# Performance work log

Measured on AMD Instinct MI355X. Metric: run time of the kernel, lower is better.

Reference implementation:

```python
import jax, jax.numpy as jnp
import numpy as np

# static config (matches torch module instantiation)
B, D, NH, HD = 2, 256, 8, 32
NL, NP, DFF = 1, 4, 1024
SHAPES = [(180, 180)]          # (H, W) per level; 180*180 = 32400
STARTS = [0]
LSRC = 32400
N_DET, N_SEG = 200, 100        # SEG_QUERY_NUM=100 -> num_seg_query=300
LQ = N_DET + N_SEG


def _lin(key, dout, din, scale=None):
    scale = scale if scale is not None else 1.0 / np.sqrt(din)
    k1, k2 = jax.random.split(key)
    return (jax.random.normal(k1, (dout, din), jnp.float32) * scale,
            jax.random.normal(k2, (dout,), jnp.float32) * 0.01)


def setup_inputs() -> dict:
    key = jax.random.key(0)
    ks = iter(jax.random.split(key, 64))
    inp = {
        'query': jax.random.normal(next(ks), (B, LQ, D), jnp.float32),
        'query_pos': jax.random.normal(next(ks), (B, LQ, D), jnp.float32),
        'src': jax.random.normal(next(ks), (B, LSRC, D), jnp.float32),
        'pos': jax.random.normal(next(ks), (B, LSRC, D), jnp.float32),
        'reference_points': jax.random.uniform(next(ks), (B, LSRC + LQ, NL, 2), jnp.float32),
        'spatial_shapes': jnp.array(SHAPES, jnp.int32),
        'level_start_index': jnp.array(STARTS, jnp.int32),
    }
    # two MSDeformAttn instances (self_attn = sa_*, cross_attn = ca_*)
    for pre in ('sa', 'ca'):
        inp[pre + '_Wv'], inp[pre + '_bv'] = _lin(next(ks), D, D)
        inp[pre + '_Woff'], inp[pre + '_boff'] = _lin(next(ks), NH * NL * NP * 2, D, scale=0.01)
        inp[pre + '_Waw'], inp[pre + '_baw'] = _lin(next(ks), NH * NL * NP, D, scale=0.01)
        inp[pre + '_Wout'], inp[pre + '_bout'] = _lin(next(ks), D, D)
    for nm in ('norm1', 'norm2', 'normq', 'qa_norm', 'norm3'):
        inp[nm + '_g'] = jnp.ones((D,), jnp.float32)
        inp[nm + '_b'] = jnp.zeros((D,), jnp.float32)
    inp['ffn1_W1'], inp['ffn1_b1'] = _lin(next(ks), DFF, D)
    inp['ffn1_W2'], inp['ffn1_b2'] = _lin(next(ks), D, DFF)
    inp['ffn3_W1'], inp['ffn3_b1'] = _lin(next(ks), DFF, D)
    inp['ffn3_W2'], inp['ffn3_b2'] = _lin(next(ks), D, DFF)
    # TCSLayer: proj(d->2d) then gate1/gate2 (d->d), sigmoid gates
    inp['tcs_Wp'], inp['tcs_bp'] = _lin(next(ks), 2 * D, D)
    inp['tcs_Wg1'], inp['tcs_bg1'] = _lin(next(ks), D, D)
    inp['tcs_Wg2'], inp['tcs_bg2'] = _lin(next(ks), D, D)
    # query self-attention (nn.MultiheadAttention): packed in_proj [3D, D]
    inp['qa_Win'], inp['qa_bin'] = _lin(next(ks), 3 * D, D)
    inp['qa_Wout'], inp['qa_bout'] = _lin(next(ks), D, D)
    return inp


def ln(x, g, b, eps=1e-5):
    m = x.mean(-1, keepdims=True)
    v = ((x - m) ** 2).mean(-1, keepdims=True)
    return (x - m) * jax.lax.rsqrt(v + eps) * g + b


def msda(q, ref, src_v, Wv, bv, Woff, boff, Waw, baw, Wout, bout):
    """MSDeformAttn: value proj -> learned offsets/weights -> bilinear sample -> out proj.
    q [B,Lq,D], ref [B,Lq,NL,2] in [0,1], src_v [B,Lin,D]."""
    Bq, Lq, _ = q.shape
    Lin = src_v.shape[1]
    value = (src_v @ Wv.T + bv).reshape(Bq, Lin, NH, HD).transpose(0, 2, 1, 3)  # [B,NH,Lin,HD]
    off = (q @ Woff.T + boff).reshape(Bq, Lq, NH, NL, NP, 2)
    aw = jax.nn.softmax((q @ Waw.T + baw).reshape(Bq, Lq, NH, NL * NP), -1)
    aw = aw.reshape(Bq, Lq, NH, NL, NP)
    norm = jnp.array([[w, h] for (h, w) in SHAPES], q.dtype)  # [NL,2] = (W,H)
    loc = ref[:, :, None, :, None, :] + off / norm[None, None, None, :, None, :]
    out = jnp.zeros((Bq, NH, Lq, HD), q.dtype)
    for l, (h, w) in enumerate(SHAPES):
        s = STARTS[l]
        v_l = value[:, :, s:s + h * w, :]
        # grid_sample align_corners=False: pixel = loc*size - 0.5, zero padding
        x = loc[:, :, :, l, :, 0] * w - 0.5  # [B,Lq,NH,NP]
        y = loc[:, :, :, l, :, 1] * h - 0.5
        x0 = jnp.floor(x); y0 = jnp.floor(y)
        lx = x - x0; ly = y - y0
        x0i = x0.astype(jnp.int32); y0i = y0.astype(jnp.int32)
        samp = jnp.zeros((Bq, NH, Lq, NP, HD), q.dtype)
        for dy, dx, wgt in ((0, 0, (1 - lx) * (1 - ly)), (0, 1, lx * (1 - ly)),
                            (1, 0, (1 - lx) * ly), (1, 1, lx * ly)):
            xi = x0i + dx; yi = y0i + dy
            valid = ((xi >= 0) & (xi < w) & (yi >= 0) & (yi < h)).astype(q.dtype)
            idx = jnp.clip(yi, 0, h - 1) * w + jnp.clip(xi, 0, w - 1)  # [B,Lq,NH,NP]
            idx_t = idx.transpose(0, 2, 1, 3).reshape(Bq, NH, Lq * NP)
            g = jnp.take_along_axis(v_l, idx_t[..., None], axis=2).reshape(Bq, NH, Lq, NP, HD)
            samp = samp + g * (wgt * valid).transpose(0, 2, 1, 3)[..., None]
        out = out + jnp.einsum('bhqpd,bqhp->bhqd', samp, aw[:, :, :, l, :])
    out = out.transpose(0, 2, 1, 3).reshape(Bq, Lq, NH * HD)
    return out @ Wout.T + bout


def mha(x, pos, Win, bin_, Wout, bout):
    qk = x + pos
    q = (qk @ Win[:D].T + bin_[:D]).reshape(*x.shape[:2], NH, HD)
    k = (qk @ Win[D:2 * D].T + bin_[D:2 * D]).reshape(*x.shape[:2], NH, HD)
    v = (x @ Win[2 * D:].T + bin_[2 * D:]).reshape(*x.shape[:2], NH, HD)
    attn = jax.nn.softmax(jnp.einsum('bqhd,bkhd->bhqk', q, k) / np.sqrt(HD), -1)
    o = jnp.einsum('bhqk,bkhd->bqhd', attn, v).reshape(*x.shape[:2], D)
    return o @ Wout.T + bout


def reference(query, query_pos, src, pos, reference_points, spatial_shapes, level_start_index,
              sa_Wv, sa_bv, sa_Woff, sa_boff, sa_Waw, sa_baw, sa_Wout, sa_bout,
              ca_Wv, ca_bv, ca_Woff, ca_boff, ca_Waw, ca_baw, ca_Wout, ca_bout,
              norm1_g, norm1_b, norm2_g, norm2_b, normq_g, normq_b,
              qa_norm_g, qa_norm_b, norm3_g, norm3_b,
              ffn1_W1, ffn1_b1, ffn1_W2, ffn1_b2,
              ffn3_W1, ffn3_b1, ffn3_W2, ffn3_b2,
              tcs_Wp, tcs_bp, tcs_Wg1, tcs_bg1, tcs_Wg2, tcs_bg2,
              qa_Win, qa_bin, qa_Wout, qa_bout):
    # deformable self-attn over BEV tokens
    src2 = msda(src + pos, reference_points[:, :LSRC], src,
                sa_Wv, sa_bv, sa_Woff, sa_boff, sa_Waw, sa_baw, sa_Wout, sa_bout)
    src = ln(src + src2, norm1_g, norm1_b)
    # FFN 1
    h = jax.nn.relu(src @ ffn1_W1.T + ffn1_b1) @ ffn1_W2.T + ffn1_b2
    src = ln(src + h, norm2_g, norm2_b)
    # TCS gating (USE_SIGMOID_GATE, not SPLIT_GATE, no OCC)
    gd, gs = jnp.split(jax.nn.gelu(src @ tcs_Wp.T + tcs_bp, approximate=False), 2, axis=-1)
    gate_det = jax.nn.sigmoid(gd @ tcs_Wg1.T + tcs_bg1)
    gate_seg = jax.nn.sigmoid(gs @ tcs_Wg2.T + tcs_bg2)
    # gated deformable cross-attn (shared cross_attn weights)
    q_det = msda(query[:, :N_DET] + query_pos[:, :N_DET],
                 reference_points[:, LSRC:LSRC + N_DET], src * gate_det,
                 ca_Wv, ca_bv, ca_Woff, ca_boff, ca_Waw, ca_baw, ca_Wout, ca_bout)
    q_seg = msda(query[:, N_DET:LQ] + query_pos[:, N_DET:LQ],
                 reference_points[:, LSRC + N_DET:LSRC + LQ], src * gate_seg,
                 ca_Wv, ca_bv, ca_Woff, ca_boff, ca_Waw, ca_baw, ca_Wout, ca_bout)
    query2 = jnp.concatenate([q_det, q_seg], 1)
    query = ln(query + query2, normq_g, normq_b)
    # query self-attention (post-norm)
    query = ln(query + mha(query, query_pos, qa_Win, qa_bin, qa_Wout, qa_bout),
               qa_norm_g, qa_norm_b)
    # FFN 3
    h3 = jax.nn.relu(query @ ffn3_W1.T + ffn3_b1) @ ffn3_W2.T + ffn3_b2
    query = ln(query + h3, norm3_g, norm3_b)
    return (query, src, gate_det, gate_seg)
```

## Files before the change

### kernel.cpp

```cpp
#include <hip/hip_runtime.h>
#include <hip/hip_bf16.h>
#include <cmath>

using bf16 = __hip_bfloat16;
typedef __bf16 bf16x8 __attribute__((ext_vector_type(8)));
typedef __bf16 bf16x4 __attribute__((ext_vector_type(4)));
typedef float f32x4 __attribute__((ext_vector_type(4)));

constexpr int D = 256;
constexpr int LSRC = 32400;
constexpr int NB = 2;
constexpr int LQ = 300;
constexpr int NDET = 200;
constexpr int MS = NB * LSRC;
constexpr int MQ = NB * LQ;
constexpr int RP_STRIDE = LSRC + LQ;
constexpr float IMGW = 180.f, IMGH = 180.f;
constexpr int IW = 180, IH = 180;

constexpr long long OFF_Q  = 0;
constexpr long long OFF_S  = (long long)MQ * D;
constexpr long long OFF_GD = OFF_S + (long long)MS * D;
constexpr long long OFF_GS = OFF_GD + (long long)MS * D;

__device__ inline void gload16(const void* g, void* l) {
  __builtin_amdgcn_global_load_lds(
      (const __attribute__((address_space(1))) void*)g,
      (__attribute__((address_space(3))) void*)l, 16, 0, 0);
}

__device__ inline int xcd_swz(int b, int nwg) {
  int q = nwg >> 3, r = nwg & 7;
  int xcd = b & 7, i = b >> 3;
  return (xcd < r ? xcd * (q + 1) : r * (q + 1) + (xcd - r) * q) + i;
}

__device__ inline bf16x8 ld8_dyn(const void* p, size_t off, bool isb) {
  if (isb) return *(const bf16x8*)((const __bf16*)p + off);
  bf16x8 r;
  const float* f = (const float*)p + off;
#pragma unroll
  for (int j = 0; j < 8; ++j) r[j] = (__bf16)f[j];
  return r;
}

__device__ inline bf16x8 ld8_add_dyn(const void* a, const void* b, size_t off, bool isb) {
  bf16x8 r;
  if (isb) {
    bf16x8 x = *(const bf16x8*)((const __bf16*)a + off);
    bf16x8 y = *(const bf16x8*)((const __bf16*)b + off);
#pragma unroll
    for (int j = 0; j < 8; ++j) r[j] = (__bf16)((float)x[j] + (float)y[j]);
  } else {
    const float* fa = (const float*)a + off;
    const float* fb = (const float*)b + off;
#pragma unroll
    for (int j = 0; j < 8; ++j) r[j] = (__bf16)(fa[j] + fb[j]);
  }
  return r;
}

__global__ void detect_kernel(const void* g, int* flag) {
  *flag = (*(const unsigned*)g == 0x3F803F80u) ? 1 : 0;
}

struct CvtEnt { const void* src; void* dst; int n; int f32out; };
struct CvtBatch { CvtEnt e[48]; int blk0[49]; int cnt; };

__global__ __launch_bounds__(256) void cvt_batch_kernel(CvtBatch cb, const int* __restrict__ flag) {
  int bid = blockIdx.x;
  int i = 0;
  for (int j = 1; j < cb.cnt; ++j) if (cb.blk0[j] <= bid) i = j;
  const CvtEnt en = cb.e[i];
  int idx = (bid - cb.blk0[i]) * 2048 + threadIdx.x * 8;
  if (idx >= en.n) return;
  const bool isb = (*flag != 0);
  if (en.f32out) {
    float v[8];
    if (isb) {
      bf16x8 x = *(const bf16x8*)((const __bf16*)en.src + idx);
#pragma unroll
      for (int j = 0; j < 8; ++j) v[j] = (float)x[j];
    } else {
      const float* s = (const float*)en.src + idx;
#pragma unroll
      for (int j = 0; j < 8; ++j) v[j] = s[j];
    }
    float* o = (float*)en.dst + idx;
#pragma unroll
    for (int j = 0; j < 8; ++j) o[j] = v[j];
  } else {
    if (isb) {
      uint4 x = *(const uint4*)((const char*)en.src + (size_t)idx * 2);
      *(uint4*)((char*)en.dst + (size_t)idx * 2) = x;
    } else {
      const float* s = (const float*)en.src + idx;
      bf16x8 o;
#pragma unroll
      for (int j = 0; j < 8; ++j) o[j] = (__bf16)s[j];
      *(bf16x8*)((__bf16*)en.dst + idx) = o;
    }
  }
}

__global__ __launch_bounds__(256) void cvt_add(const void* __restrict__ a, const void* __restrict__ b,
                                               const int* __restrict__ flag,
                                               bf16* __restrict__ a_b, bf16* __restrict__ b_b,
                                               bf16* __restrict__ sum, int n8) {
  int i = blockIdx.x * 256 + threadIdx.x;
  if (i >= n8) return;
  const bool isb = (*flag != 0);
  float va[8], vb[8];
  bf16x8 ab, bb;
  if (isb) {
    ab = *(const bf16x8*)((const __bf16*)a + (size_t)i * 8);
    bb = *(const bf16x8*)((const __bf16*)b + (size_t)i * 8);
#pragma unroll
    for (int j = 0; j < 8; ++j) { va[j] = (float)ab[j]; vb[j] = (float)bb[j]; }
  } else {
    const float* pa = (const float*)a + (size_t)i * 8;
    const float* pb = (const float*)b + (size_t)i * 8;
#pragma unroll
    for (int j = 0; j < 8; ++j) { va[j] = pa[j]; vb[j] = pb[j]; ab[j] = (__bf16)va[j]; bb[j] = (__bf16)vb[j]; }
  }
  bf16x8 sb;
#pragma unroll
  for (int j = 0; j < 8; ++j) sb[j] = (__bf16)(va[j] + vb[j]);
  if (a_b) *(bf16x8*)((__bf16*)a_b + (size_t)i * 8) = ab;
  if (b_b) *(bf16x8*)((__bf16*)b_b + (size_t)i * 8) = bb;
  *(bf16x8*)((__bf16*)sum + (size_t)i * 8) = sb;
}

template<int ACT, int OUTB, int RESM>
__global__ __launch_bounds__(256) void gemm_bt(
    const bf16* __restrict__ A, int lda,
    const bf16* __restrict__ Wt,
    const bf16* __restrict__ bias,
    const void* __restrict__ res,
    void* __restrict__ out, int ldo,
    int M, int N, int K)
{
  __shared__ __bf16 As[2][64 * 32];
  __shared__ __bf16 Bs[2][64 * 32];
  const int gy = gridDim.y;
  const int nwg = gridDim.x * gy;
  const int t = xcd_swz(blockIdx.y * gridDim.x + blockIdx.x, nwg);
  const int m0 = (t / gy) * 64;
  const int n0 = (t % gy) * 64;
  const int tid = threadIdx.x;
  const int lane = tid & 63, wid = tid >> 6;
  const int wm = (wid >> 1) * 32, wn = (wid & 1) * 32;
  f32x4 acc[2][2] = {};
  const int lr = tid >> 2;
  const int lc = (tid & 3) * 8;
  const bf16* Ap = A + (size_t)(m0 + lr) * lda + lc;
  const bf16* Wp = Wt + (size_t)(n0 + lr) * K + lc;
  const int fr = lane & 15, ks = (lane >> 4) * 8;

  for (int k0 = 0; k0 < K; k0 += 64) {
    __syncthreads();
#pragma unroll
    for (int kk = 0; kk < 2; ++kk) {
      const int kc = k0 + kk * 32;
      gload16((const __bf16*)Ap + kc, &As[kk][8 * tid]);
      gload16((const __bf16*)Wp + kc, &Bs[kk][8 * tid]);
    }
    __syncthreads();
#pragma unroll
    for (int kk = 0; kk < 2; ++kk) {
      bf16x8 a0 = *(const bf16x8*)&As[kk][(wm + fr) * 32 + ks];
      bf16x8 a1 = *(const bf16x8*)&As[kk][(wm + 16 + fr) * 32 + ks];
      bf16x8 b0 = *(const bf16x8*)&Bs[kk][(wn + fr) * 32 + ks];
      bf16x8 b1 = *(const bf16x8*)&Bs[kk][(wn + 16 + fr) * 32 + ks];
      acc[0][0] = __builtin_amdgcn_mfma_f32_16x16x32_bf16(a0, b0, acc[0][0], 0, 0, 0);
      acc[0][1] = __builtin_amdgcn_mfma_f32_16x16x32_bf16(a0, b1, acc[0][1], 0, 0, 0);
      acc[1][0] = __builtin_amdgcn_mfma_f32_16x16x32_bf16(a1, b0, acc[1][0], 0, 0, 0);
      acc[1][1] = __builtin_amdgcn_mfma_f32_16x16x32_bf16(a1, b1, acc[1][1], 0, 0, 0);
    }
  }

  const int rq = (lane >> 4) * 4;
#pragma unroll
  for (int fm = 0; fm < 2; ++fm)
#pragma unroll
  for (int fn = 0; fn < 2; ++fn) {
    int ncol = n0 + wn + fn * 16 + fr;
    if (ncol >= N) continue;
    float bvs = (float)bias[ncol];
#pragma unroll
    for (int i = 0; i < 4; ++i) {
      int mrow = m0 + wm + fm * 16 + rq + i;
      if (mrow >= M) continue;
      float v = acc[fm][fn][i] + bvs;
      if (RESM == 1) v += (float)((const bf16*)res)[(size_t)mrow * ldo + ncol];
      else if (RESM == 2) v += ((const float*)res)[(size_t)mrow * ldo + ncol];
      if (ACT == 1) v = fmaxf(v, 0.f);
      else if (ACT == 2) v = 0.5f * v * (1.f + erff(v * 0.7071067811865476f));
      else if (ACT == 3) v = 1.f / (1.f + __expf(-v));
      if (OUTB) ((bf16*)out)[(size_t)mrow * ldo + ncol] = (bf16)v;
      else ((float*)out)[(size_t)mrow * ldo + ncol] = v;
    }
  }
}

template<int ADYN>
__global__ __launch_bounds__(256) void gemm_bt_add(
    const void* __restrict__ A1, const void* __restrict__ A2, int lda,
    const bf16* __restrict__ Wt, const bf16* __restrict__ bias,
    float* __restrict__ out, int ldo, int M, int N, int K,
    const int* __restrict__ flagp)
{
  __shared__ __bf16 As[2][64 * 32];
  __shared__ __bf16 Bs[2][64 * 32];
  const int gy = gridDim.y;
  const int nwg = gridDim.x * gy;
  const int t = xcd_swz(blockIdx.y * gridDim.x + blockIdx.x, nwg);
  const int m0 = (t / gy) * 64;
  const int n0 = (t % gy) * 64;
  const int tid = threadIdx.x;
  const int lane = tid & 63, wid = tid >> 6;
  const int wm = (wid >> 1) * 32, wn = (wid & 1) * 32;
  f32x4 acc[2][2] = {};
  const int lr = tid >> 2;
  const int lc = (tid & 3) * 8;
  const int ar = min(m0 + lr, M - 1);
  const size_t abase = (size_t)ar * lda + lc;
  const bf16* Wp = Wt + (size_t)(n0 + lr) * K + lc;
  const bool isb = ADYN ? (*flagp != 0) : true;
  const int fr = lane & 15, ks = (lane >> 4) * 8;

  for (int k0 = 0; k0 < K; k0 += 64) {
    bf16x8 av[2];
#pragma unroll
    for (int kk = 0; kk < 2; ++kk)
      av[kk] = ld8_add_dyn(A1, A2, abase + k0 + kk * 32, isb);
    __syncthreads();
#pragma unroll
    for (int kk = 0; kk < 2; ++kk) {
      *(bf16x8*)&As[kk][8 * tid] = av[kk];
      gload16((const __bf16*)Wp + k0 + kk * 32, &Bs[kk][8 * tid]);
    }
    __syncthreads();
#pragma unroll
    for (int kk = 0; kk < 2; ++kk) {
      bf16x8 a0 = *(const bf16x8*)&As[kk][(wm + fr) * 32 + ks];
      bf16x8 a1 = *(const bf16x8*)&As[kk][(wm + 16 + fr) * 32 + ks];
      bf16x8 b0 = *(const bf16x8*)&Bs[kk][(wn + fr) * 32 + ks];
      bf16x8 b1 = *(const bf16x8*)&Bs[kk][(wn + 16 + fr) * 32 + ks];
      acc[0][0] = __builtin_amdgcn_mfma_f32_16x16x32_bf16(a0, b0, acc[0][0], 0, 0, 0);
      acc[0][1] = __builtin_amdgcn_mfma_f32_16x16x32_bf16(a0, b1, acc[0][1], 0, 0, 0);
      acc[1][0] = __builtin_amdgcn_mfma_f32_16x16x32_bf16(a1, b0, acc[1][0], 0, 0, 0);
      acc[1][1] = __builtin_amdgcn_mfma_f32_16x16x32_bf16(a1, b1, acc[1][1], 0, 0, 0);
    }
  }

  const int rq = (lane >> 4) * 4;
#pragma unroll
  for (int fm = 0; fm < 2; ++fm)
#pragma unroll
  for (int fn = 0; fn < 2; ++fn) {
    int ncol = n0 + wn + fn * 16 + fr;
    if (ncol >= N) continue;
    float bvs = (float)bias[ncol];
#pragma unroll
    for (int i = 0; i < 4; ++i) {
      int mrow = m0 + wm + fm * 16 + rq + i;
      if (mrow >= M) continue;
      out[(size_t)mrow * ldo + ncol] = acc[fm][fn][i] + bvs;
    }
  }
}

template<int ACT, int OUTB, int RESM, int EMIT>
__global__ __launch_bounds__(256) void gemm128(
    const bf16* __restrict__ A, int lda,
    const bf16* __restrict__ Wt,
    const bf16* __restrict__ bias,
    const void* __restrict__ res,
    void* __restrict__ out, int ldo,
    int M, int N, int K,
    const int* __restrict__ flagp, void* __restrict__ ob, long long eoff)
{
  __shared__ __bf16 As[2][128 * 32];
  __shared__ __bf16 Bs[2][128 * 32];
  const int gy = gridDim.y;
  const int nwg = gridDim.x * gy;
  const int t = xcd_swz(blockIdx.y * gridDim.x + blockIdx.x, nwg);
  const int m0 = (t / gy) * 128;
  const int n0 = (t % gy) * 128;
  const int tid = threadIdx.x;
  const int lane = tid & 63, wid = tid >> 6;
  const int wr = (wid >> 1) * 64, wc = (wid & 1) * 64;
  const int fr = lane & 15, ks = (lane >> 4) * 8;
  f32x4 acc[4][4] = {};

  const int srow = tid >> 2;
  const int scol = (tid & 3) * 8;
  const bf16* Ap0 = A + (size_t)(m0 + srow) * lda + scol;
  const bf16* Ap1 = A + (size_t)(m0 + 64 + srow) * lda + scol;
  const bf16* Bp0 = Wt + (size_t)(n0 + srow) * K + scol;
  const bf16* Bp1 = Wt + (size_t)(n0 + 64 + srow) * K + scol;

  for (int k0 = 0; k0 < K; k0 += 64) {
    __syncthreads();
#pragma unroll
    for (int kk = 0; kk < 2; ++kk) {
      const int kc = k0 + kk * 32;
      gload16((const __bf16*)Ap0 + kc, &As[kk][8 * tid]);
      gload16((const __bf16*)Ap1 + kc, &As[kk][64 * 32 + 8 * tid]);
      gload16((const __bf16*)Bp0 + kc, &Bs[kk][8 * tid]);
      gload16((const __bf16*)Bp1 + kc, &Bs[kk][64 * 32 + 8 * tid]);
    }
    __syncthreads();
#pragma unroll
    for (int kk = 0; kk < 2; ++kk) {
      bf16x8 af[4], bfv[4];
#pragma unroll
      for (int m = 0; m < 4; ++m) af[m]  = *(const bf16x8*)&As[kk][(wr + m * 16 + fr) * 32 + ks];
#pragma unroll
      for (int n = 0; n < 4; ++n) bfv[n] = *(const bf16x8*)&Bs[kk][(wc + n * 16 + fr) * 32 + ks];
#pragma unroll
      for (int m = 0; m < 4; ++m)
#pragma unroll
        for (int n = 0; n < 4; ++n)
          acc[m][n] = __builtin_amdgcn_mfma_f32_16x16x32_bf16(af[m], bfv[n], acc[m][n], 0, 0, 0);
    }
  }

  const bool isb = EMIT ? (*flagp != 0) : false;
  const int rq = (lane >> 4) * 4;
#pragma unroll
  for (int m = 0; m < 4; ++m) {
    const int mb = m0 + wr + m * 16 + rq;
#pragma unroll
    for (int n = 0; n < 4; ++n) {
      const int ncol = n0 + wc + n * 16 + fr;
      const float bvs = (float)bias[ncol];
#pragma unroll
      for (int i = 0; i < 4; ++i) {
        const int mrow = mb + i;
        if (mrow >= M) continue;
        float v = acc[m][n][i] + bvs;
        if (RESM == 1) v += (float)((const bf16*)res)[(size_t)mrow * ldo + ncol];
        else if (RESM == 2) v += ((const float*)res)[(size_t)mrow * ldo + ncol];
        if (ACT == 1) v = fmaxf(v, 0.f);
        else if (ACT == 2) v = 0.5f * v * (1.f + erff(v * 0.7071067811865476f));
        else if (ACT == 3) v = 1.f / (1.f + __expf(-v));
        if (OUTB) ((bf16*)out)[(size_t)mrow * ldo + ncol] = (bf16)v;
        else ((float*)out)[(size_t)mrow * ldo + ncol] = v;
        if (EMIT) {
          long long eo = eoff + (long long)mrow * ldo + ncol;
          if (isb) ((__bf16*)ob)[eo] = (__bf16)v;
          else ((float*)ob)[eo] = v;
        }
      }
    }
  }
}

template<int OP, int SDYN>
__global__ __launch_bounds__(256) void gemm128_rs(
    const void* __restrict__ S, const bf16* __restrict__ G0, const bf16* __restrict__ G1,
    int lda,
    const bf16* __restrict__ Wt, const bf16* __restrict__ bias,
    bf16* __restrict__ out0, bf16* __restrict__ out1, int ldo,
    int M, int N, int K, const int* __restrict__ flagp)
{
  __shared__ __bf16 As[2][128 * 32];
  __shared__ __bf16 Bs[2][128 * 32];
  const bf16* G = blockIdx.z ? G1 : G0;
  bf16* out = blockIdx.z ? out1 : out0;
  const int gy = gridDim.y;
  const int nwg = gridDim.x * gy;
  const int t = xcd_swz(blockIdx.y * gridDim.x + blockIdx.x, nwg);
  const int m0 = (t / gy) * 128;
  const int n0 = (t % gy) * 128;
  const int tid = threadIdx.x;
  const int lane = tid & 63, wid = tid >> 6;
  const int wr = (wid >> 1) * 64, wc = (wid & 1) * 64;
  const int fr = lane & 15, ks = (lane >> 4) * 8;
  f32x4 acc[4][4] = {};

  const int srow = tid >> 2;
  const int scol = (tid & 3) * 8;
  const int r0 = min(m0 + srow, M - 1);
  const int r1 = min(m0 + 64 + srow, M - 1);
  const size_t s0off = (size_t)r0 * lda + scol;
  const size_t s1off = (size_t)r1 * lda + scol;
  const bf16* Bp0 = Wt + (size_t)(n0 + srow) * K + scol;
  const bf16* Bp1 = Wt + (size_t)(n0 + 64 + srow) * K + scol;
  const bool isb = SDYN ? (*flagp != 0) : true;

  for (int k0 = 0; k0 < K; k0 += 64) {
    bf16x8 a0[2], a1[2];
#pragma unroll
    for (int kk = 0; kk < 2; ++kk) {
      const int kc = kk * 32 + k0;
      bf16x8 s0 = ld8_dyn(S, s0off + kc, isb);
      bf16x8 s1 = ld8_dyn(S, s1off + kc, isb);
      if (OP == 1) {
        bf16x8 g0 = *(const bf16x8*)((const __bf16*)G + s0off + kc);
        bf16x8 g1 = *(const bf16x8*)((const __bf16*)G + s1off + kc);
#pragma unroll
        for (int j = 0; j < 8; ++j) {
          a0[kk][j] = (__bf16)((float)s0[j] * (float)g0[j]);
          a1[kk][j] = (__bf16)((float)s1[j] * (float)g1[j]);
        }
      } else {
        a0[kk] = s0;
        a1[kk] = s1;
      }
    }
    __syncthreads();
#pragma unroll
    for (int kk = 0; kk < 2; ++kk) {
      const int kc = kk * 32 + k0;
      *(bf16x8*)&As[kk][8 * tid] = a0[kk];
      *(bf16x8*)&As[kk][64 * 32 + 8 * tid] = a1[kk];
      gload16((const __bf16*)Bp0 + kc, &Bs[kk][8 * tid]);
      gload16((const __bf16*)Bp1 + kc, &Bs[kk][64 * 32 + 8 * tid]);
    }
    __syncthreads();
#pragma unroll
    for (int kk = 0; kk < 2; ++kk) {
      bf16x8 af[4], bfv[4];
#pragma unroll
      for (int m = 0; m < 4; ++m) af[m]  = *(const bf16x8*)&As[kk][(wr + m * 16 + fr) * 32 + ks];
#pragma unroll
      for (int n = 0; n < 4; ++n) bfv[n] = *(const bf16x8*)&Bs[kk][(wc + n * 16 + fr) * 32 + ks];
#pragma unroll
      for (int m = 0; m < 4; ++m)
#pragma unroll
        for (int n = 0; n < 4; ++n)
          acc[m][n] = __builtin_amdgcn_mfma_f32_16x16x32_bf16(af[m], bfv[n], acc[m][n], 0, 0, 0);
    }
  }

  const int rq = (lane >> 4) * 4;
#pragma unroll
  for (int m = 0; m < 4; ++m) {
    const int mb = m0 + wr + m * 16 + rq;
#pragma unroll
    for (int n = 0; n < 4; ++n) {
      const int ncol = n0 + wc + n * 16 + fr;
      const float bvs = (float)bias[ncol];
#pragma unroll
      for (int i = 0; i < 4; ++i) {
        const int mrow = mb + i;
        if (mrow >= M) continue;
        out[(size_t)mrow * ldo + ncol] = (bf16)(acc[m][n][i] + bvs);
      }
    }
  }
}

template<int RESM, int EMIT, int OUTF>
__global__ __launch_bounds__(256) void gemm_ln(
    const bf16* __restrict__ A, int lda,
    const bf16* __restrict__ Wt,
    const bf16* __restrict__ bias,
    const void* __restrict__ res,
    const bf16* __restrict__ g, const bf16* __restrict__ b,
    bf16* __restrict__ outb, float* __restrict__ outf,
    int M, int K,
    const int* __restrict__ flagp, void* __restrict__ ob, long long eoff)
{
  __shared__ __bf16 As[2][64 * 32];
  __shared__ __bf16 Bs[2][256 * 32];
  __shared__ float redS[4][64], redQ[4][64];
  const int m0 = blockIdx.x * 64;
  const int tid = threadIdx.x, lane = tid & 63, wid = tid >> 6;
  const int wc = wid * 64;
  const int fr = lane & 15, ks = (lane >> 4) * 8;
  f32x4 acc[4][4] = {};
  const int srow = tid >> 2, scol = (tid & 3) * 8;
  const bf16* Ap = A + (size_t)(m0 + srow) * lda + scol;
  const bf16* Bp = Wt + (size_t)srow * K + scol;

  for (int k0 = 0; k0 < K; k0 += 64) {
    __syncthreads();
#pragma unroll
    for (int kk = 0; kk < 2; ++kk) {
      const int kc = k0 + kk * 32;
      gload16((const __bf16*)Ap + kc, &As[kk][8 * tid]);
#pragma unroll
      for (int j = 0; j < 4; ++j)
        gload16((const __bf16*)(Bp + (size_t)j * 64 * K) + kc, &Bs[kk][j * 64 * 32 + 8 * tid]);
    }
    __syncthreads();
#pragma unroll
    for (int kk = 0; kk < 2; ++kk) {
      bf16x8 af[4], bfv[4];
#pragma unroll
      for (int m = 0; m < 4; ++m) af[m]  = *(const bf16x8*)&As[kk][(m * 16 + fr) * 32 + ks];
#pragma unroll
      for (int n = 0; n < 4; ++n) bfv[n] = *(const bf16x8*)&Bs[kk][(wc + n * 16 + fr) * 32 + ks];
#pragma unroll
      for (int m = 0; m < 4; ++m)
#pragma unroll
        for (int n = 0; n < 4; ++n)
          acc[m][n] = __builtin_amdgcn_mfma_f32_16x16x32_bf16(af[m], bfv[n], acc[m][n], 0, 0, 0);
    }
  }

  const int rq = (lane >> 4) * 4;
  const bool fb = (EMIT || RESM == 3) ? (*flagp != 0) : false;
  float bvals[4], gvals[4], bb2[4];
#pragma unroll
  for (int n = 0; n < 4; ++n) {
    bvals[n] = (float)bias[wc + n * 16 + fr];
    gvals[n] = (float)g[wc + n * 16 + fr];
    bb2[n]   = (float)b[wc + n * 16 + fr];
  }
#pragma unroll
  for (int m = 0; m < 4; ++m)
#pragma unroll
  for (int i = 0; i < 4; ++i) {
    const int mrow = m0 + m * 16 + rq + i;
    const int rr = mrow < M ? mrow : M - 1;
#pragma unroll
    for (int n = 0; n < 4; ++n) {
      const size_t ri = (size_t)rr * 256 + wc + n * 16 + fr;
      float r;
      if (RESM == 1) r = (float)((const bf16*)res)[ri];
      else if (RESM == 2) r = ((const float*)res)[ri];
      else r = fb ? (float)((const bf16*)res)[ri] : ((const float*)res)[ri];
      acc[m][n][i] += bvals[n] + r;
    }
    float s = acc[m][0][i] + acc[m][1][i] + acc[m][2][i] + acc[m][3][i];
    float q = acc[m][0][i] * acc[m][0][i] + acc[m][1][i] * acc[m][1][i]
            + acc[m][2][i] * acc[m][2][i] + acc[m][3][i] * acc[m][3][i];
#pragma unroll
    for (int off = 1; off <= 8; off <<= 1) {
      s += __shfl_xor(s, off);
      q += __shfl_xor(q, off);
    }
    if (fr == 0) { redS[wid][m * 16 + rq + i] = s; redQ[wid][m * 16 + rq + i] = q; }
  }
  __syncthreads();
#pragma unroll
  for (int m = 0; m < 4; ++m)
#pragma unroll
  for (int i = 0; i < 4; ++i) {
    const int rl = m * 16 + rq + i;
    const int mrow = m0 + rl;
    if (mrow >= M) continue;
    float ts = redS[0][rl] + redS[1][rl] + redS[2][rl] + redS[3][rl];
    float tq = redQ[0][rl] + redQ[1][rl] + redQ[2][rl] + redQ[3][rl];
    float mean = ts * (1.f / 256.f);
    float var = tq * (1.f / 256.f) - mean * mean;
    float rstd = rsqrtf(var + 1e-5f);
#pragma unroll
    for (int n = 0; n < 4; ++n) {
      const int col = wc + n * 16 + fr;
      float y = (acc[m][n][i] - mean) * rstd * gvals[n] + bb2[n];
      if (outb) outb[(size_t)mrow * 256 + col] = (bf16)y;
      if (OUTF) outf[(size_t)mrow * 256 + col] = y;
      if (EMIT) {
        long long eo = eoff + (long long)mrow * 256 + col;
        if (fb) ((__bf16*)ob)[eo] = (__bf16)y;
        else ((float*)ob)[eo] = y;
      }
    }
  }
}

__global__ __launch_bounds__(256) void msda_sample4(
    const float* __restrict__ oa,
    const float* __restrict__ rpf, int rp_base, int qcnt4, int lqrow, int split,
    const bf16* __restrict__ valA, const bf16* __restrict__ valB,
    bf16* __restrict__ out, int swz) {
  int blk = blockIdx.x;
  if (swz) blk = xcd_swz(blk, gridDim.x);
  int b = blk / qcnt4;
  int wid = threadIdx.x >> 6, lane = threadIdx.x & 63;
  int qi = (blk % qcnt4) * 4 + wid;
  size_t row = (size_t)b * lqrow + qi;
  int h = lane >> 3, d0 = (lane & 7) * 4;
  const bf16* val = (qi < split) ? valA : valB;
  const __bf16* vb = (const __bf16*)val + (size_t)b * LSRC * 256 + h * 32 + d0;
  float rx = rpf[((size_t)b * RP_STRIDE + rp_base + qi) * 2 + 0];
  float ry = rpf[((size_t)b * RP_STRIDE + rp_base + qi) * 2 + 1];
  const float* offp = oa + row * 96 + h * 8;
  const float* awp  = oa + row * 96 + 64 + h * 4;
  float a0 = awp[0], a1 = awp[1], a2 = awp[2], a3 = awp[3];
  float mx = fmaxf(fmaxf(a0, a1), fmaxf(a2, a3));
  float e0 = __expf(a0 - mx), e1 = __expf(a1 - mx), e2 = __expf(a2 - mx), e3 = __expf(a3 - mx);
  float rs = 1.f / (e0 + e1 + e2 + e3);
  float aws[4] = { e0 * rs, e1 * rs, e2 * rs, e3 * rs };
  float o0 = 0.f, o1 = 0.f, o2 = 0.f, o3 = 0.f;
#pragma unroll
  for (int p = 0; p < 4; ++p) {
    float x = rx * IMGW + offp[p * 2 + 0] - 0.5f;
    float y = ry * IMGH + offp[p * 2 + 1] - 0.5f;
    float x0f = floorf(x), y0f = floorf(y);
    float lx = x - x0f, ly = y - y0f;
    int x0 = (int)x0f, y0 = (int)y0f;
#pragma unroll
    for (int dy = 0; dy < 2; ++dy)
#pragma unroll
    for (int dx = 0; dx < 2; ++dx) {
      int xi = x0 + dx, yi = y0 + dy;
      if (xi >= 0 && xi < IW && yi >= 0 && yi < IH) {
        float wgt = aws[p] * (dx ? lx : 1.f - lx) * (dy ? ly : 1.f - ly);
        bf16x4 gv = *(const bf16x4*)(vb + (size_t)(yi * IW + xi) * 256);
        o0 += wgt * (float)gv[0]; o1 += wgt * (float)gv[1];
        o2 += wgt * (float)gv[2]; o3 += wgt * (float)gv[3];
      }
    }
  }
  bf16x4 ov;
  ov[0] = (__bf16)o0; ov[1] = (__bf16)o1; ov[2] = (__bf16)o2; ov[3] = (__bf16)o3;
  *(bf16x4*)((__bf16*)out + row * 256 + h * 32 + d0) = ov;
}

__global__ __launch_bounds__(256) void mha_attn(
    const float* __restrict__ qk,
    const float* __restrict__ v,
    bf16* __restrict__ o) {
  __shared__ float probs[4][304];
  int bh = blockIdx.x / 75;
  int j  = blockIdx.x % 75;
  int b = bh >> 3, h = bh & 7;
  int wid = threadIdx.x >> 6, lane = threadIdx.x & 63;
  const float scale = 0.17677669529663687f;
  int q = j * 4 + wid;
  const float* qv = qk + ((size_t)(b * 300 + q)) * 512 + h * 32;
  float p[5];
  float mx = -1e30f;
#pragma unroll
  for (int s5 = 0; s5 < 5; ++s5) {
    int k = lane + 64 * s5;
    float sacc = -1e30f;
    if (k < 300) {
      const float* kv = qk + ((size_t)(b * 300 + k)) * 512 + 256 + h * 32;
      float sd = 0.f;
#pragma unroll
      for (int dd = 0; dd < 32; ++dd) sd += qv[dd] * kv[dd];
      sacc = sd * scale;
    }
    p[s5] = sacc;
    mx = fmaxf(mx, sacc);
  }
#pragma unroll
  for (int off = 32; off; off >>= 1) mx = fmaxf(mx, __shfl_xor(mx, off));
  float ssum = 0.f;
#pragma unroll
  for (int s5 = 0; s5 < 5; ++s5) {
    p[s5] = (p[s5] > -1e29f) ? __expf(p[s5] - mx) : 0.f;
    ssum += p[s5];
  }
#pragma unroll
  for (int off = 32; off; off >>= 1) ssum += __shfl_xor(ssum, off);
  float rinv = 1.f / ssum;
#pragma unroll
  for (int s5 = 0; s5 < 5; ++s5) {
    int k = lane + 64 * s5;
    if (k < 300) probs[wid][k] = p[s5] * rinv;
  }
  __syncthreads();
  {
    int d = lane & 31, half = lane >> 5;
    float acc = 0.f;
    for (int k = half * 150; k < half * 150 + 150; ++k)
      acc += probs[wid][k] * v[((size_t)(b * 300 + k)) * 256 + h * 32 + d];
    acc += __shfl_xor(acc, 32);
    if (lane < 32) o[((size_t)(b * 300 + q)) * 256 + h * 32 + d] = (bf16)acc;
  }
}

extern "C" void kernel_launch(void* const* d_in, const int* in_sizes, int n_in,
                              void* d_out, int out_size, void* d_ws, size_t ws_size,
                              hipStream_t stream) {
  (void)n_in; (void)out_size; (void)ws_size;
  const size_t SZ = (size_t)MS * D * sizeof(bf16);

  char* w = (char*)d_ws;
  auto carve = [&](size_t bytes) { char* p = w; w += (bytes + 255) & ~(size_t)255; return p; };

  int*   flag = (int*)carve(256);
  float* rp_f = (float*)carve((size_t)NB * RP_STRIDE * 2 * 4);

  bf16* wb[51] = {};
  bf16* wcat_s = nullptr; bf16* bcat_s = nullptr;
  bf16* wcat_q = nullptr; bf16* bcat_q = nullptr;
  for (int i = 7; i <= 50; ++i) {
    if (i == 9)       { wcat_s = (bf16*)carve((size_t)96 * 256 * 2); wb[9]  = wcat_s; }
    else if (i == 10) { bcat_s = (bf16*)carve(96 * 2);               wb[10] = bcat_s; }
    else if (i == 11) { wb[11] = wcat_s + 64 * 256; }
    else if (i == 12) { wb[12] = bcat_s + 64; }
    else if (i == 17) { wcat_q = (bf16*)carve((size_t)96 * 256 * 2); wb[17] = wcat_q; }
    else if (i == 18) { bcat_q = (bf16*)carve(96 * 2);               wb[18] = bcat_q; }
    else if (i == 19) { wb[19] = wcat_q + 64 * 256; }
    else if (i == 20) { wb[20] = bcat_q + 64; }
    else wb[i] = (bf16*)carve((size_t)in_sizes[i] * 2);
  }

  bf16* query_b     = (bf16*)carve((size_t)MQ * D * 2);
  bf16* query_pos_b = (bf16*)carve((size_t)MQ * D * 2);
  bf16* qx_q        = (bf16*)carve((size_t)MQ * D * 2);
  bf16* att_q       = (bf16*)carve((size_t)MQ * D * 2);
  bf16* q_x         = (bf16*)carve((size_t)MQ * D * 2);
  bf16* mha_o       = (bf16*)carve((size_t)MQ * D * 2);
  bf16* lnq_b       = (bf16*)carve((size_t)MQ * D * 2);
  bf16* qh          = (bf16*)carve((size_t)MQ * 1024 * 2);
  float* qoffawb    = (float*)carve((size_t)MQ * 96 * 4);
  float* q_res      = (float*)carve((size_t)MQ * D * 4);
  float* qk_f       = (float*)carve((size_t)MQ * 512 * 4);
  float* v_f        = (float*)carve((size_t)MQ * D * 4);

  char* A = carve(SZ);
  char* B = carve(SZ);
  char* C = carve(SZ);
  char* Dd = carve(SZ);
  char* E = carve(SZ);
  carve(512 * 1024);

  const bf16* query     = (const bf16*)d_in[0];
  const bf16* query_pos = (const bf16*)d_in[1];
  const void* src       = d_in[2];
  const void* pos       = d_in[3];

  dim3 blk(256);
  const int GS64  = (MS + 63) / 64;
  const int GQ64  = (MQ + 63) / 64;
  const int G128  = (MS + 127) / 128;

  detect_kernel<<<1, 1, 0, stream>>>(d_in[23], flag);
  {
    CvtBatch cb{};
    int nb = 0, cnt = 0;
    auto addcvt = [&](const void* s, void* dst, int n, int f32o) {
      cb.e[cnt] = { s, dst, n, f32o };
      cb.blk0[cnt] = nb;
      nb += (n + 2047) / 2048;
      ++cnt;
    };
    addcvt(d_in[4], rp_f, in_sizes[4], 1);
    for (int i = 7; i <= 50; ++i) addcvt(d_in[i], wb[i], in_sizes[i], 0);
    cb.cnt = cnt;
    cvt_batch_kernel<<<nb, blk, 0, stream>>>(cb, flag);
  }
  cvt_add<<<MQ * D / 8 / 256, blk, 0, stream>>>(query, query_pos, flag, query_b, query_pos_b, qx_q, MQ * D / 8);

  float* offawb = (float*)B;
  bf16*  val    = (bf16*)Dd;
  gemm_bt_add<1><<<dim3(GS64,2), blk, 0, stream>>>(src, pos, 256, wb[9], wb[10], offawb, 96, MS, 96, 256, flag);
  gemm128_rs<0,1><<<dim3(G128,2,1), blk, 0, stream>>>(src, nullptr, nullptr, 256, wb[7], wb[8], val, nullptr, 256, MS, 256, 256, flag);
  bf16* samp = (bf16*)C;
  msda_sample4<<<NB * (LSRC / 4), blk, 0, stream>>>(offawb, rp_f, 0, LSRC / 4, LSRC, 1 << 30, val, val, samp, 1);
  bf16* lnx = (bf16*)C;
  gemm_ln<3,0,0><<<GS64, blk, 0, stream>>>(samp, 256, wb[13], wb[14], src, wb[23], wb[24],
                                           lnx, nullptr, MS, 256, flag, nullptr, 0);

  bf16* srcout = (bf16*)A;
  {
    const int CH = MS / 2;
    const int GC128 = (CH + 127) / 128;
    const int GC64  = (CH + 63) / 64;
    bf16* hid = (bf16*)Dd;
    for (int c = 0; c < 2; ++c) {
      size_t ro = (size_t)c * CH * 256;
      gemm128<1,1,0,0><<<dim3(GC128,8), blk, 0, stream>>>(lnx + ro, 256, wb[33], wb[34], nullptr, hid, 1024, CH, 1024, 256, nullptr, nullptr, 0);
      gemm_ln<1,1,0><<<GC64, blk, 0, stream>>>(hid, 1024, wb[35], wb[36], lnx + ro, wb[25], wb[26],
                                               srcout + ro, nullptr, CH, 1024, flag, d_out, OFF_S + (long long)ro);
    }
  }

  bf16* proj = (bf16*)Dd;
  bf16* gdt  = (bf16*)B;
  bf16* gst  = (bf16*)C;
  gemm128<2,1,0,0><<<dim3(G128,4), blk, 0, stream>>>(srcout, 256, wb[41], wb[42], nullptr, proj, 512, MS, 512, 256, nullptr, nullptr, 0);
  gemm128<3,1,0,1><<<dim3(G128,2), blk, 0, stream>>>(proj,       512, wb[43], wb[44], nullptr, gdt, 256, MS, 256, 256, flag, d_out, OFF_GD);
  gemm128<3,1,0,1><<<dim3(G128,2), blk, 0, stream>>>(proj + 256, 512, wb[45], wb[46], nullptr, gst, 256, MS, 256, 256, flag, d_out, OFF_GS);

  gemm_bt<0,0,0><<<dim3(GQ64,2), blk, 0, stream>>>(qx_q, 256, wb[17], wb[18], nullptr, qoffawb, 96, MQ, 96, 256);

  bf16* val_det = (bf16*)Dd;
  bf16* val_seg = (bf16*)E;
  gemm128_rs<1,0><<<dim3(G128,2,2), blk, 0, stream>>>(srcout, gdt, gst, 256, wb[15], wb[16],
                                                      val_det, val_seg, 256, MS, 256, 256, nullptr);
  msda_sample4<<<NB * (LQ / 4), blk, 0, stream>>>(qoffawb, rp_f, LSRC, LQ / 4, LQ, NDET, val_det, val_seg, att_q, 0);

  gemm_ln<1,0,1><<<GQ64, blk, 0, stream>>>(att_q, 256, wb[21], wb[22], query_b, wb[27], wb[28],
                                           q_x, q_res, MQ, 256, nullptr, nullptr, 0);

  gemm_bt_add<0><<<dim3(GQ64,8), blk, 0, stream>>>(q_x, query_pos_b, 256, wb[47], wb[48], qk_f, 512, MQ, 512, 256, flag);
  gemm_bt<0,0,0><<<dim3(GQ64,4), blk, 0, stream>>>(q_x, 256, wb[47] + (size_t)512 * 256, wb[48] + 512, nullptr, v_f, 256, MQ, 256, 256);
  mha_attn<<<NB * 8 * 75, blk, 0, stream>>>(qk_f, v_f, mha_o);
  gemm_ln<2,0,1><<<GQ64, blk, 0, stream>>>(mha_o, 256, wb[49], wb[50], q_res, wb[29], wb[30],
                                           q_x, q_res, MQ, 256, nullptr, nullptr, 0);

  gemm_bt<1,1,0><<<dim3(GQ64,16), blk, 0, stream>>>(q_x, 256, wb[37], wb[38], nullptr, qh, 1024, MQ, 1024, 256);
  gemm_ln<2,1,0><<<GQ64, blk, 0, stream>>>(qh, 1024, wb[39], wb[40], q_res, wb[31], wb[32],
                                           lnq_b, nullptr, MQ, 1024, flag, d_out, OFF_Q);
}
```

Baseline: 741.6 us.

## Merge gate GEMMs into one launch, read gates from output buffer, add occupancy hints

The two sigmoid gate GEMMs become one launch (z selects det or seg), and it writes only to the final output buffer instead of also storing bf16 copies. The gated value GEMM now reads the gates back from the output buffer, in fp32 or bf16 depending on the runtime flag. Separately, all GEMM kernels get launch_bounds min-blocks of 2 to push for higher occupancy. This removes one launch and the duplicate gate writes, but the value GEMM may now read fp32 gates (twice the bytes), and the tighter register limit risks spills.

```diff
diff --git a/kernel.cpp b/kernel.cpp
--- a/kernel.cpp
+++ b/kernel.cpp
@@ -42,6 +42,18 @@
 #pragma unroll
   for (int j = 0; j < 8; ++j) r[j] = (__bf16)f[j];
   return r;
+}
+
+__device__ inline void ld8f_dyn(const void* p, size_t off, bool isb, float* o) {
+  if (isb) {
+    bf16x8 x = *(const bf16x8*)((const __bf16*)p + off);
+#pragma unroll
+    for (int j = 0; j < 8; ++j) o[j] = (float)x[j];
+  } else {
+    const float* f = (const float*)p + off;
+#pragma unroll
+    for (int j = 0; j < 8; ++j) o[j] = f[j];
+  }
 }
 
 __device__ inline bf16x8 ld8_add_dyn(const void* a, const void* b, size_t off, bool isb) {
@@ -132,7 +144,7 @@
 }
 
 template<int ACT, int OUTB, int RESM>
-__global__ __launch_bounds__(256) void gemm_bt(
+__global__ __launch_bounds__(256, 2) void gemm_bt(
     const bf16* __restrict__ A, int lda,
     const bf16* __restrict__ Wt,
     const bf16* __restrict__ bias,
@@ -204,7 +216,7 @@
 }
 
 template<int ADYN>
-__global__ __launch_bounds__(256) void gemm_bt_add(
+__global__ __launch_bounds__(256, 2) void gemm_bt_add(
     const void* __restrict__ A1, const void* __restrict__ A2, int lda,
     const bf16* __restrict__ Wt, const bf16* __restrict__ bias,
     float* __restrict__ out, int ldo, int M, int N, int K,
@@ -272,7 +284,7 @@
 }
 
 template<int ACT, int OUTB, int RESM, int EMIT>
-__global__ __launch_bounds__(256) void gemm128(
+__global__ __launch_bounds__(256, 2) void gemm128(
     const bf16* __restrict__ A, int lda,
     const bf16* __restrict__ Wt,
     const bf16* __restrict__ bias,
@@ -358,9 +370,90 @@
   }
 }
 
-template<int OP, int SDYN>
-__global__ __launch_bounds__(256) void gemm128_rs(
-    const void* __restrict__ S, const bf16* __restrict__ G0, const bf16* __restrict__ G1,
+__global__ __launch_bounds__(256, 2) void gemm_gate2(
+    const bf16* __restrict__ proj,
+    const bf16* __restrict__ W0, const bf16* __restrict__ b0,
+    const bf16* __restrict__ W1, const bf16* __restrict__ b1,
+    void* __restrict__ ob, long long eo0, long long eo1,
+    int M, const int* __restrict__ flagp)
+{
+  constexpr int K = 256, ldaP = 512;
+  __shared__ __bf16 As[2][128 * 32];
+  __shared__ __bf16 Bs[2][128 * 32];
+  const bf16* Wt = blockIdx.z ? W1 : W0;
+  const bf16* bias = blockIdx.z ? b1 : b0;
+  const long long eoff = blockIdx.z ? eo1 : eo0;
+  const bf16* A = proj + (blockIdx.z ? 256 : 0);
+  const int gy = gridDim.y;
+  const int nwg = gridDim.x * gy;
+  const int t = xcd_swz(blockIdx.y * gridDim.x + blockIdx.x, nwg);
+  const int m0 = (t / gy) * 128;
+  const int n0 = (t % gy) * 128;
+  const int tid = threadIdx.x;
+  const int lane = tid & 63, wid = tid >> 6;
+  const int wr = (wid >> 1) * 64, wc = (wid & 1) * 64;
+  const int fr = lane & 15, ks = (lane >> 4) * 8;
+  f32x4 acc[4][4] = {};
+
+  const int srow = tid >> 2;
+  const int scol = (tid & 3) * 8;
+  const bf16* Ap0 = A + (size_t)(m0 + srow) * ldaP + scol;
+  const bf16* Ap1 = A + (size_t)(m0 + 64 + srow) * ldaP + scol;
+  const bf16* Bp0 = Wt + (size_t)(n0 + srow) * K + scol;
+  const bf16* Bp1 = Wt + (size_t)(n0 + 64 + srow) * K + scol;
+
+  for (int k0 = 0; k0 < K; k0 += 64) {
+    __syncthreads();
+#pragma unroll
+    for (int kk = 0; kk < 2; ++kk) {
+      const int kc = k0 + kk * 32;
+      gload16((const __bf16*)Ap0 + kc, &As[kk][8 * tid]);
+      gload16((const __bf16*)Ap1 + kc, &As[kk][64 * 32 + 8 * tid]);
+      gload16((const __bf16*)Bp0 + kc, &Bs[kk][8 * tid]);
+      gload16((const __bf16*)Bp1 + kc, &Bs[kk][64 * 32 + 8 * tid]);
+    }
+    __syncthreads();
+#pragma unroll
+    for (int kk = 0; kk < 2; ++kk) {
+      bf16x8 af[4], bfv[4];
+#pragma unroll
+      for (int m = 0; m < 4; ++m) af[m]  = *(const bf16x8*)&As[kk][(wr + m * 16 + fr) * 32 + ks];
+#pragma unroll
+      for (int n = 0; n < 4; ++n) bfv[n] = *(const bf16x8*)&Bs[kk][(wc + n * 16 + fr) * 32 + ks];
+#pragma unroll
+      for (int m = 0; m < 4; ++m)
+#pragma unroll
+        for (int n = 0; n < 4; ++n)
+          acc[m][n] = __builtin_amdgcn_mfma_f32_16x16x32_bf16(af[m], bfv[n], acc[m][n], 0, 0, 0);
+    }
+  }
+
+  const bool isb = (*flagp != 0);
+  const int rq = (lane >> 4) * 4;
+#pragma unroll
+  for (int m = 0; m < 4; ++m) {
+    const int mb = m0 + wr + m * 16 + rq;
+#pragma unroll
+    for (int n = 0; n < 4; ++n) {
+      const int ncol = n0 + wc + n * 16 + fr;
+      const float bvs = (float)bias[ncol];
+#pragma unroll
+      for (int i = 0; i < 4; ++i) {
+        const int mrow = mb + i;
+        if (mrow >= M) continue;
+        float v = 1.f / (1.f + __expf(-(acc[m][n][i] + bvs)));
+        long long eo = eoff + (long long)mrow * 256 + ncol;
+        if (isb) ((__bf16*)ob)[eo] = (__bf16)v;
+        else ((float*)ob)[eo] = v;
+      }
+    }
+  }
+}
+
+template<int OP, int SDYN, int GDYN>
+__global__ __launch_bounds__(256, 2) void gemm128_rs(
+    const void* __restrict__ S, const void* __restrict__ gbase,
+    long long geo0, long long geo1,
     int lda,
     const bf16* __restrict__ Wt, const bf16* __restrict__ bias,
     bf16* __restrict__ out0, bf16* __restrict__ out1, int ldo,
@@ -368,7 +461,7 @@
 {
   __shared__ __bf16 As[2][128 * 32];
   __shared__ __bf16 Bs[2][128 * 32];
-  const bf16* G = blockIdx.z ? G1 : G0;
+  const long long geo = blockIdx.z ? geo1 : geo0;
   bf16* out = blockIdx.z ? out1 : out0;
   const int gy = gridDim.y;
   const int nwg = gridDim.x * gy;
@@ -389,22 +482,25 @@
   const size_t s1off = (size_t)r1 * lda + scol;
   const bf16* Bp0 = Wt + (size_t)(n0 + srow) * K + scol;
   const bf16* Bp1 = Wt + (size_t)(n0 + 64 + srow) * K + scol;
-  const bool isb = SDYN ? (*flagp != 0) : true;
+  const bool isb = (SDYN || GDYN) ? (*flagp != 0) : true;
+  const bool isbS = SDYN ? isb : true;
+  const bool isbG = GDYN ? isb : true;
 
   for (int k0 = 0; k0 < K; k0 += 64) {
     bf16x8 a0[2], a1[2];
 #pragma unroll
     for (int kk = 0; kk < 2; ++kk) {
       const int kc = kk * 32 + k0;
-      bf16x8 s0 = ld8_dyn(S, s0off + kc, isb);
-      bf16x8 s1 = ld8_dyn(S, s1off + kc, isb);
+      bf16x8 s0 = ld8_dyn(S, s0off + kc, isbS);
+      bf16x8 s1 = ld8_dyn(S, s1off + kc, isbS);
       if (OP == 1) {
-        bf16x8 g0 = *(const bf16x8*)((const __bf16*)G + s0off + kc);
-        bf16x8 g1 = *(const bf16x8*)((const __bf16*)G + s1off + kc);
+        float g0[8], g1[8];
+        ld8f_dyn(gbase, (size_t)geo + s0off + kc, isbG, g0);
+        ld8f_dyn(gbase, (size_t)geo + s1off + kc, isbG, g1);
 #pragma unroll
         for (int j = 0; j < 8; ++j) {
-          a0[kk][j] = (__bf16)((float)s0[j] * (float)g0[j]);
-          a1[kk][j] = (__bf16)((float)s1[j] * (float)g1[j]);
+          a0[kk][j] = (__bf16)((float)s0[j] * g0[j]);
+          a1[kk][j] = (__bf16)((float)s1[j] * g1[j]);
         }
       } else {
         a0[kk] = s0;
@@ -455,7 +551,7 @@
 }
 
 template<int RESM, int EMIT, int OUTF>
-__global__ __launch_bounds__(256) void gemm_ln(
+__global__ __launch_bounds__(256, 2) void gemm_ln(
     const bf16* __restrict__ A, int lda,
     const bf16* __restrict__ Wt,
     const bf16* __restrict__ bias,
@@ -746,7 +842,7 @@
   float* offawb = (float*)B;
   bf16*  val    = (bf16*)Dd;
   gemm_bt_add<1><<<dim3(GS64,2), blk, 0, stream>>>(src, pos, 256, wb[9], wb[10], offawb, 96, MS, 96, 256, flag);
-  gemm128_rs<0,1><<<dim3(G128,2,1), blk, 0, stream>>>(src, nullptr, nullptr, 256, wb[7], wb[8], val, nullptr, 256, MS, 256, 256, flag);
+  gemm128_rs<0,1,0><<<dim3(G128,2,1), blk, 0, stream>>>(src, nullptr, 0, 0, 256, wb[7], wb[8], val, nullptr, 256, MS, 256, 256, flag);
   bf16* samp = (bf16*)C;
   msda_sample4<<<NB * (LSRC / 4), blk, 0, stream>>>(offawb, rp_f, 0, LSRC / 4, LSRC, 1 << 30, val, val, samp, 1);
   bf16* lnx = (bf16*)C;
@@ -768,18 +864,17 @@
   }
 
   bf16* proj = (bf16*)Dd;
-  bf16* gdt  = (bf16*)B;
-  bf16* gst  = (bf16*)C;
   gemm128<2,1,0,0><<<dim3(G128,4), blk, 0, stream>>>(srcout, 256, wb[41], wb[42], nullptr, proj, 512, MS, 512, 256, nullptr, nullptr, 0);
-  gemm128<3,1,0,1><<<dim3(G128,2), blk, 0, stream>>>(proj,       512, wb[43], wb[44], nullptr, gdt, 256, MS, 256, 256, flag, d_out, OFF_GD);
-  gemm128<3,1,0,1><<<dim3(G128,2), blk, 0, stream>>>(proj + 256, 512, wb[45], wb[46], nullptr, gst, 256, MS, 256, 256, flag, d_out, OFF_GS);
+  gemm_gate2<<<dim3(G128,2,2), blk, 0, stream>>>(proj, wb[43], wb[44], wb[45], wb[46],
+                                                 d_out, OFF_GD, OFF_GS, MS, flag);
 
   gemm_bt<0,0,0><<<dim3(GQ64,2), blk, 0, stream>>>(qx_q, 256, wb[17], wb[18], nullptr, qoffawb, 96, MQ, 96, 256);
 
   bf16* val_det = (bf16*)Dd;
   bf16* val_seg = (bf16*)E;
-  gemm128_rs<1,0><<<dim3(G128,2,2), blk, 0, stream>>>(srcout, gdt, gst, 256, wb[15], wb[16],
-                                                      val_det, val_seg, 256, MS, 256, 256, nullptr);
+  gemm128_rs<1,0,1><<<dim3(G128,2,2), blk, 0, stream>>>(srcout, d_out, OFF_GD, OFF_GS, 256,
+                                                        wb[15], wb[16], val_det, val_seg, 256,
+                                                        MS, 256, 256, flag);
   msda_sample4<<<NB * (LQ / 4), blk, 0, stream>>>(qoffawb, rp_f, LSRC, LQ / 4, LQ, NDET, val_det, val_seg, att_q, 0);
 
   gemm_ln<1,0,1><<<GQ64, blk, 0, stream>>>(att_q, 256, wb[21], wb[22], query_b, wb[27], wb[28],
```

After: 665.7 us, median of 2. -10.2%, faster.
